# Kernel optimization log

Measured on AMD Instinct MI355X. Metric: run time of the kernel, lower is better.

The kernel has to match this reference:

```python
import jax, jax.numpy as jnp
import numpy as np

E, H, I, T, K = 8, 2048, 1024, 4096, 2
GROUP = 32


def dequant_int4(packed, scale, group):
    """packed: [E, R, C//2] ints in [0,256) holding two 4-bit values per byte.
    scale: [E, R, C//group]. Returns fp32 [E, R, C] with w = (nibble - 8) * scale."""
    lo = (packed & 0xF) - 8          # even columns
    hi = ((packed >> 4) & 0xF) - 8   # odd columns
    e, r, ch = packed.shape
    w = jnp.stack([lo, hi], axis=-1).reshape(e, r, 2 * ch).astype(jnp.float32)
    w = w.reshape(e, r, -1, group) * scale[..., None]
    return w.reshape(e, r, 2 * ch)


def setup_inputs() -> dict:
    key = jax.random.key(0)
    ks = jax.random.split(key, 6)
    x = jax.random.normal(ks[0], (T, H), dtype=jnp.float32)
    w1 = jax.random.randint(ks[1], (E, 2 * I, H // 2), 0, 256, dtype=jnp.int32)
    w1_scale = jax.random.uniform(ks[2], (E, 2 * I, H // GROUP), dtype=jnp.float32) * 0.02
    w2 = jax.random.randint(ks[3], (E, H, I // 2), 0, 256, dtype=jnp.int32)
    w2_scale = jax.random.uniform(ks[4], (E, H, I // GROUP), dtype=jnp.float32) * 0.02
    logits = jax.random.normal(ks[5], (T, E), dtype=jnp.float32)
    top_vals, top_idx = jax.lax.top_k(logits, K)
    expert_weights = jax.nn.softmax(top_vals, axis=-1)   # [T, K]
    expert_indices = top_idx.astype(jnp.int32)           # [T, K]
    return {"x": x, "w1": w1, "w1_scale": w1_scale, "w2": w2,
            "w2_scale": w2_scale, "expert_weights": expert_weights,
            "expert_indices": expert_indices, "top_k": K}


def reference(x, w1, w1_scale, w2, w2_scale, expert_weights, expert_indices, top_k):
    inter = w2.shape[2] * 2
    W1 = dequant_int4(w1, w1_scale, GROUP)   # [E, 2I, H]
    W2 = dequant_int4(w2, w2_scale, GROUP)   # [E, H, I]
    y13 = jnp.einsum('th,erh->etr', x, W1)   # [E, T, 2I]
    gate, up = y13[..., :inter], y13[..., inter:]
    h = jax.nn.silu(gate) * up               # [E, T, I] SwiGLU
    y = jnp.einsum('eti,ehi->eth', h, W2)    # [E, T, H]
    t_ids = jnp.arange(x.shape[0])[:, None]  # [T, 1]
    sel = y[expert_indices, t_ids, :]        # [T, K, H]
    return jnp.einsum('tkh,tk->th', sel, expert_weights)
```

## Files before the change

kernel.cpp:

```cpp
#include <hip/hip_runtime.h>
#include <cstdint>
#include <cstddef>

typedef unsigned int u32;
typedef unsigned short u16;
typedef __bf16 bf16x8 __attribute__((ext_vector_type(8)));
typedef float f32x4 __attribute__((ext_vector_type(4)));
typedef u16 u16x8 __attribute__((ext_vector_type(8)));

static constexpr int T_TOK = 4096;
static constexpr int HID   = 2048;
static constexpr int INTER = 1024;
static constexpr int NEXP  = 8;
static constexpr int TOPK  = 2;
static constexpr int SLOT_CAP = 10240;
static constexpr int NT_M = 40;

static constexpr int M_TOT    = 16;
static constexpr int M_CUR    = 17;
static constexpr int M_DONE   = 40;
static constexpr int M_TOK    = 96;
static constexpr int M_SLOTOF = 96 + SLOT_CAP;

__device__ __forceinline__ u16 f2bf(float f) {
  u32 u = __builtin_bit_cast(u32, f);
  u32 r = (u + 0x7fffu + ((u >> 16) & 1u)) >> 16;
  return (u16)r;
}
__device__ __forceinline__ float bf2f(u16 h) {
  return __builtin_bit_cast(float, (u32)h << 16);
}

__device__ __forceinline__ void spin_ge(int* p, int target) {
  while (__hip_atomic_load(p, __ATOMIC_RELAXED, __HIP_MEMORY_SCOPE_AGENT) < target)
    __builtin_amdgcn_s_sleep(8);
  __builtin_amdgcn_fence(__ATOMIC_ACQUIRE, "agent");
}
__device__ __forceinline__ void bump(int* p, int tid) {
  __syncthreads();
  if (tid == 0)
    __hip_atomic_fetch_add(p, 1, __ATOMIC_RELEASE, __HIP_MEMORY_SCOPE_AGENT);
}

__global__ void router_count(const int* __restrict__ eidx, int* __restrict__ meta) {
  __shared__ int cnt[NEXP];
  const int tid = threadIdx.x;
  if (tid < NEXP) cnt[tid] = 0;
  __syncthreads();
  for (int i = tid; i < T_TOK * TOPK; i += 256) atomicAdd(&cnt[eidx[i]], 1);
  __syncthreads();
  if (tid == 0) {
    int off = 0;
    for (int e = 0; e < NEXP; ++e) {
      int c = cnt[e];
      meta[e] = c;
      meta[8 + e] = off;
      meta[M_CUR + e] = off;
      off += (c + 255) & ~255;
    }
    meta[M_TOT] = off;
  }
}

__global__ void init_k(int* __restrict__ meta) {
  const int i = blockIdx.x * 256 + threadIdx.x;
  if (i < SLOT_CAP) meta[M_TOK + i] = 0;
  if (i >= 25 && i < 80) meta[i] = 0;
}

__global__ void router_assign(const int* __restrict__ eidx, int* __restrict__ meta) {
  const int t = blockIdx.x * 256 + threadIdx.x;
  if (t >= T_TOK) return;
  int* cursors = meta + M_CUR;
  int* toklist = meta + M_TOK;
  int* slotof  = meta + M_SLOTOF;
  for (int k = 0; k < TOPK; ++k) {
    const int e = eidx[t * TOPK + k];
    const int pos = atomicAdd(&cursors[e], 1);
    toklist[pos] = t * 2 + k;
    slotof[t * 2 + k] = pos;
  }
}

template <int CPR>
__device__ __forceinline__ void deq1(const int* __restrict__ p, const float* __restrict__ s,
                                     u16* __restrict__ w, int gid) {
  const int row = gid / CPR;
  const int cid = gid % CPR;
  const int4 pk = *(const int4*)(p + (size_t)gid * 4);
  const float sc = s[(size_t)row * (CPR / 4) + (cid >> 2)];
  int v[4] = {pk.x, pk.y, pk.z, pk.w};
  u16x8 o;
#pragma unroll
  for (int b = 0; b < 4; ++b) {
    o[2 * b]     = f2bf((float)((v[b] & 15) - 8) * sc);
    o[2 * b + 1] = f2bf((float)(((v[b] >> 4) & 15) - 8) * sc);
  }
  *(u16x8*)(w + (size_t)gid * 8) = o;
}

__global__ void prep_k(const int* __restrict__ w1, const float* __restrict__ w1s,
                       const int* __restrict__ w2, const float* __restrict__ w2s,
                       const float* __restrict__ x, u16* __restrict__ W1b,
                       u16* __restrict__ W2b, u16* __restrict__ xs,
                       const int* __restrict__ meta) {
  const int blk = blockIdx.x;
  if (blk < 16384) {
    deq1<256>(w1, w1s, W1b, blk * 256 + threadIdx.x);
  } else if (blk < 24576) {
    deq1<128>(w2, w2s, W2b, (blk - 16384) * 256 + threadIdx.x);
  } else {
    const int slot = blk - 24576;
    const int tok = meta[M_TOK + slot] >> 1;
    const float* src = x + (size_t)tok * HID + threadIdx.x * 8;
    const float4 a = *(const float4*)src;
    const float4 b = *(const float4*)(src + 4);
    u16x8 o;
    o[0] = f2bf(a.x); o[1] = f2bf(a.y); o[2] = f2bf(a.z); o[3] = f2bf(a.w);
    o[4] = f2bf(b.x); o[5] = f2bf(b.y); o[6] = f2bf(b.z); o[7] = f2bf(b.w);
    *(u16x8*)(xs + (size_t)slot * HID + threadIdx.x * 8) = o;
  }
}

template <int KT, bool G1M>
__device__ void gemm_body(const u16* __restrict__ A, const u16* __restrict__ Be,
                          u16* __restrict__ Cout, u16* lds, int slot0, int nt, int tid) {
  static constexpr int NT = KT / 64;
  char* ldsB = (char*)lds;

  const u16* asrc[4];
  const u16* bsrc[4];
#pragma unroll
  for (int j = 0; j < 4; ++j) {
    const int L = j * 8192 + tid * 16;
    const int S = L >> 10;
    int o = L & 1023;
    o ^= ((o >> 7) & 3) << 4;
    const int r = (S >> 1) * 16 + (o >> 6);
    const int cb = (S & 1) * 64 + (o & 63);
    asrc[j] = A + (size_t)(slot0 + r) * KT + (cb >> 1);
    int brow;
    if (G1M) {
      const int g = r >> 6, j6 = r & 63;
      brow = nt * 128 + g * 32 + (j6 & 31) + ((j6 >> 5) << 10);
    } else {
      brow = nt * 256 + r;
    }
    bsrc[j] = Be + (size_t)brow * KT + (cb >> 1);
  }

#define STAGE(kt_, c_)                                                                \
  do {                                                                                \
    char* dA_ = ldsB + (c_) * 65536;                                                  \
    char* dB_ = dA_ + 32768;                                                          \
    _Pragma("unroll") for (int j = 0; j < 4; ++j)                                     \
        __builtin_amdgcn_global_load_lds(                                             \
            (const __attribute__((address_space(1))) void*)(asrc[j] + (kt_) * 64),    \
            (__attribute__((address_space(3))) void*)(dA_ + j * 8192 + tid * 16),     \
            16, 0, 0);                                                                \
    _Pragma("unroll") for (int j = 0; j < 4; ++j)                                     \
        __builtin_amdgcn_global_load_lds(                                             \
            (const __attribute__((address_space(1))) void*)(bsrc[j] + (kt_) * 64),    \
            (__attribute__((address_space(3))) void*)(dB_ + j * 8192 + tid * 16),     \
            16, 0, 0);                                                                \
  } while (0)

  const int lane = tid & 63;
  const int wid = tid >> 6;
  const int wm = (wid >> 2) * 128;
  const int wn = (wid & 3) * 64;
  const int fr = lane & 15;
  const int qq = lane >> 4;
  const int swz = (qq * 16) ^ (((fr >> 1) & 3) << 4);

  const int abase = (wm >> 4) * 2048 + fr * 64 + swz;
  const int bbase = 32768 + (wn >> 4) * 2048 + fr * 64 + swz;

  f32x4 acc[8][4];
#pragma unroll
  for (int m = 0; m < 8; ++m)
#pragma unroll
    for (int n = 0; n < 4; ++n) acc[m][n] = (f32x4)0.0f;

#define COMPUTE(c_)                                                                   \
  do {                                                                                \
    const char* bb_ = ldsB + (c_) * 65536;                                            \
    bf16x8 bfr_[4][2];                                                                \
    _Pragma("unroll") for (int nf = 0; nf < 4; ++nf)                                  \
        _Pragma("unroll") for (int ks = 0; ks < 2; ++ks)                              \
            bfr_[nf][ks] = *(const bf16x8*)(bb_ + bbase + nf * 2048 + ks * 1024);     \
    _Pragma("unroll") for (int mh = 0; mh < 2; ++mh) {                                \
      bf16x8 af_[4][2];                                                               \
      _Pragma("unroll") for (int mf = 0; mf < 4; ++mf)                                \
          _Pragma("unroll") for (int ks = 0; ks < 2; ++ks)                            \
              af_[mf][ks] = *(const bf16x8*)(bb_ + abase + mh * 8192 + mf * 2048 +    \
                                             ks * 1024);                              \
      __builtin_amdgcn_s_setprio(1);                                                  \
      _Pragma("unroll") for (int mf = 0; mf < 4; ++mf)                                \
          _Pragma("unroll") for (int nf = 0; nf < 4; ++nf)                            \
              _Pragma("unroll") for (int ks = 0; ks < 2; ++ks)                        \
                  acc[mh * 4 + mf][nf] = __builtin_amdgcn_mfma_f32_16x16x32_bf16(     \
                      af_[mf][ks], bfr_[nf][ks], acc[mh * 4 + mf][nf], 0, 0, 0);      \
      __builtin_amdgcn_s_setprio(0);                                                  \
    }                                                                                 \
  } while (0)

  STAGE(0, 0);
#pragma unroll 1
  for (int kt = 0; kt < NT; kt += 2) {
    asm volatile("s_waitcnt vmcnt(0)" ::: "memory");
    __builtin_amdgcn_s_barrier();
    __builtin_amdgcn_sched_barrier(0);
    if (kt + 1 < NT) STAGE(kt + 1, 1);
    COMPUTE(0);
    asm volatile("s_waitcnt vmcnt(0)" ::: "memory");
    __builtin_amdgcn_s_barrier();
    __builtin_amdgcn_sched_barrier(0);
    if (kt + 2 < NT) STAGE(kt + 2, 0);
    COMPUTE(1);
  }
#undef STAGE
#undef COMPUTE

  if (G1M) {
    const int g = wid & 3;
#pragma unroll
    for (int mi = 0; mi < 8; ++mi)
#pragma unroll
      for (int n = 0; n < 2; ++n)
#pragma unroll
        for (int jj = 0; jj < 4; ++jj) {
          const float gv = acc[mi][n][jj];
          const float uv = acc[mi][n + 2][jj];
          const float hv = gv / (1.0f + __expf(-gv)) * uv;
          const int row = slot0 + wm + mi * 16 + qq * 4 + jj;
          Cout[(size_t)row * INTER + nt * 128 + g * 32 + n * 16 + fr] = f2bf(hv);
        }
  } else {
#pragma unroll
    for (int mi = 0; mi < 8; ++mi)
#pragma unroll
      for (int jj = 0; jj < 4; ++jj) {
        const int row = slot0 + wm + mi * 16 + qq * 4 + jj;
        const int col = nt * 256 + wn + fr;
#pragma unroll
        for (int n = 0; n < 4; ++n)
          Cout[(size_t)row * HID + col + n * 16] = f2bf(acc[mi][n][jj]);
      }
  }
}

__device__ __forceinline__ void run_g1(const u16* xs, const u16* W1b, u16* hbuf,
                                       int* meta, u16* lds, int mt, int nt, int tid) {
  const int slot0 = mt * 256;
  if (slot0 < meta[M_TOT]) {
    int e = 0;
#pragma unroll
    for (int i = 1; i < NEXP; ++i) e += (slot0 >= meta[8 + i]);
    gemm_body<2048, true>(xs, W1b + (size_t)e * 2048 * 2048, hbuf, lds, slot0, nt, tid);
  }
  bump(&meta[M_DONE + mt], tid);
}

__device__ __forceinline__ void run_g2(const u16* hbuf, const u16* W2b, u16* ys,
                                       int* meta, u16* lds, int mt, int nt, int tid) {
  const int slot0 = mt * 256;
  if (slot0 >= meta[M_TOT]) return;
  int e = 0;
#pragma unroll
  for (int i = 1; i < NEXP; ++i) e += (slot0 >= meta[8 + i]);
  if (tid == 0) spin_ge(&meta[M_DONE + mt], 8);
  __syncthreads();
  gemm_body<1024, false>(hbuf, W2b + (size_t)e * 2048 * 1024, ys, lds, slot0, nt, tid);
}

__global__ __launch_bounds__(512, 2) void gemm_static(
    const u16* __restrict__ xs, const u16* __restrict__ W1b,
    const u16* __restrict__ W2b, u16* __restrict__ hbuf, u16* __restrict__ ys,
    int* __restrict__ meta) {
  __shared__ u16 lds[2 * 32768];
  const int tid = threadIdx.x;
  const int b = blockIdx.x;

  run_g1(xs, W1b, hbuf, meta, lds, b & 31, b >> 5, tid);
  if (b < 64) {
    run_g1(xs, W1b, hbuf, meta, lds, 32 + (b & 7), b >> 3, tid);
    run_g2(hbuf, W2b, ys, meta, lds, 32 + (b & 7), b >> 3, tid);
  } else {
    const int x = b & 7, q = (b - 64) >> 3;
    {
      const int k = q;
      run_g2(hbuf, W2b, ys, meta, lds, x + 8 * (k & 3), k >> 2, tid);
    }
    if (q < 8) {
      const int k = q + 24;
      run_g2(hbuf, W2b, ys, meta, lds, x + 8 * (k & 3), k >> 2, tid);
    }
  }
}

__global__ void combine_k(const u16* __restrict__ ys, const float* __restrict__ ew,
                          const int* __restrict__ meta, float* __restrict__ out) {
  const int idx = blockIdx.x * 256 + threadIdx.x;
  const int t = idx >> 8;
  const int pos = (idx & 255) * 8;
  const int* slotof = meta + M_SLOTOF;
  const int s0 = slotof[t * 2];
  const int s1 = slotof[t * 2 + 1];
  const float w0 = ew[t * 2];
  const float w1 = ew[t * 2 + 1];
  const u16x8 v0 = *(const u16x8*)(ys + (size_t)s0 * HID + pos);
  const u16x8 v1 = *(const u16x8*)(ys + (size_t)s1 * HID + pos);
  float* dst = out + (size_t)t * HID + pos;
  float4 o0, o1;
  o0.x = w0 * bf2f(v0[0]) + w1 * bf2f(v1[0]);
  o0.y = w0 * bf2f(v0[1]) + w1 * bf2f(v1[1]);
  o0.z = w0 * bf2f(v0[2]) + w1 * bf2f(v1[2]);
  o0.w = w0 * bf2f(v0[3]) + w1 * bf2f(v1[3]);
  o1.x = w0 * bf2f(v0[4]) + w1 * bf2f(v1[4]);
  o1.y = w0 * bf2f(v0[5]) + w1 * bf2f(v1[5]);
  o1.z = w0 * bf2f(v0[6]) + w1 * bf2f(v1[6]);
  o1.w = w0 * bf2f(v0[7]) + w1 * bf2f(v1[7]);
  *(float4*)dst = o0;
  *(float4*)(dst + 4) = o1;
}

extern "C" void kernel_launch(void* const* d_in, const int* in_sizes, int n_in,
                              void* d_out, int out_size, void* d_ws, size_t ws_size,
                              hipStream_t stream) {
  const float* x    = (const float*)d_in[0];
  const int*   w1   = (const int*)d_in[1];
  const float* w1s  = (const float*)d_in[2];
  const int*   w2   = (const int*)d_in[3];
  const float* w2s  = (const float*)d_in[4];
  const float* ew   = (const float*)d_in[5];
  const int*   eidx = (const int*)d_in[6];
  float* out = (float*)d_out;

  char* ws = (char*)d_ws;
  const size_t OFF_W1B  = 0;
  const size_t OFF_W2B  = 67108864;
  const size_t OFF_XS   = 100663296;
  const size_t OFF_H    = 142606336;
  const size_t OFF_META = 163577856;
  const size_t NEED     = 163708928;
  if (ws_size < NEED) return;

  u16* W1b  = (u16*)(ws + OFF_W1B);
  u16* W2b  = (u16*)(ws + OFF_W2B);
  u16* xs   = (u16*)(ws + OFF_XS);
  u16* hbuf = (u16*)(ws + OFF_H);
  int* meta = (int*)(ws + OFF_META);

  router_count<<<1, 256, 0, stream>>>(eidx, meta);
  init_k<<<SLOT_CAP / 256, 256, 0, stream>>>(meta);
  router_assign<<<T_TOK / 256, 256, 0, stream>>>(eidx, meta);

  prep_k<<<34816, 256, 0, stream>>>(w1, w1s, w2, w2s, x, W1b, W2b, xs, meta);

  gemm_static<<<256, 512, 0, stream>>>(xs, W1b, W2b, hbuf, xs, meta);

  combine_k<<<(T_TOK * HID) / (256 * 8), 256, 0, stream>>>(xs, ew, meta, out);
}
```

Baseline: 254.3 us.

## Fuse int4 weight dequant into GEMM B-tile staging, drop prep pass

Removes the separate pass that dequantized all expert weights to bf16 in workspace. The GEMM now loads packed int4 words and scales into registers, dequantizes them, and writes bf16 B tiles directly into LDS, with a reworked double-buffer schedule. The x gather becomes a per-token kernel that writes each token's bf16 row to both of its slots. This saves the large bf16 weight write and reread, but adds VALU dequant work and register pressure inside the GEMM loop, and B loads lose the async global-to-LDS path. Each weight tile is also dequantized once per M-tile rather than once overall.

```diff
diff --git a/kernel.cpp b/kernel.cpp
--- a/kernel.cpp
+++ b/kernel.cpp
@@ -82,54 +82,33 @@
   }
 }
 
-template <int CPR>
-__device__ __forceinline__ void deq1(const int* __restrict__ p, const float* __restrict__ s,
-                                     u16* __restrict__ w, int gid) {
-  const int row = gid / CPR;
-  const int cid = gid % CPR;
-  const int4 pk = *(const int4*)(p + (size_t)gid * 4);
-  const float sc = s[(size_t)row * (CPR / 4) + (cid >> 2)];
-  int v[4] = {pk.x, pk.y, pk.z, pk.w};
+__global__ void xprep_k(const float* __restrict__ x, const int* __restrict__ meta,
+                        u16* __restrict__ xs) {
+  const int t = blockIdx.x;
+  const int col = threadIdx.x * 8;
+  const float* src = x + (size_t)t * HID + col;
+  const float4 a = *(const float4*)src;
+  const float4 b = *(const float4*)(src + 4);
   u16x8 o;
-#pragma unroll
-  for (int b = 0; b < 4; ++b) {
-    o[2 * b]     = f2bf((float)((v[b] & 15) - 8) * sc);
-    o[2 * b + 1] = f2bf((float)(((v[b] >> 4) & 15) - 8) * sc);
-  }
-  *(u16x8*)(w + (size_t)gid * 8) = o;
-}
-
-__global__ void prep_k(const int* __restrict__ w1, const float* __restrict__ w1s,
-                       const int* __restrict__ w2, const float* __restrict__ w2s,
-                       const float* __restrict__ x, u16* __restrict__ W1b,
-                       u16* __restrict__ W2b, u16* __restrict__ xs,
-                       const int* __restrict__ meta) {
-  const int blk = blockIdx.x;
-  if (blk < 16384) {
-    deq1<256>(w1, w1s, W1b, blk * 256 + threadIdx.x);
-  } else if (blk < 24576) {
-    deq1<128>(w2, w2s, W2b, (blk - 16384) * 256 + threadIdx.x);
-  } else {
-    const int slot = blk - 24576;
-    const int tok = meta[M_TOK + slot] >> 1;
-    const float* src = x + (size_t)tok * HID + threadIdx.x * 8;
-    const float4 a = *(const float4*)src;
-    const float4 b = *(const float4*)(src + 4);
-    u16x8 o;
-    o[0] = f2bf(a.x); o[1] = f2bf(a.y); o[2] = f2bf(a.z); o[3] = f2bf(a.w);
-    o[4] = f2bf(b.x); o[5] = f2bf(b.y); o[6] = f2bf(b.z); o[7] = f2bf(b.w);
-    *(u16x8*)(xs + (size_t)slot * HID + threadIdx.x * 8) = o;
-  }
+  o[0] = f2bf(a.x); o[1] = f2bf(a.y); o[2] = f2bf(a.z); o[3] = f2bf(a.w);
+  o[4] = f2bf(b.x); o[5] = f2bf(b.y); o[6] = f2bf(b.z); o[7] = f2bf(b.w);
+  const int s0 = meta[M_SLOTOF + 2 * t];
+  const int s1 = meta[M_SLOTOF + 2 * t + 1];
+  *(u16x8*)(xs + (size_t)s0 * HID + col) = o;
+  *(u16x8*)(xs + (size_t)s1 * HID + col) = o;
 }
 
 template <int KT, bool G1M>
-__device__ void gemm_body(const u16* __restrict__ A, const u16* __restrict__ Be,
-                          u16* __restrict__ Cout, u16* lds, int slot0, int nt, int tid) {
+__device__ void gemm_body(const u16* __restrict__ A, const int* __restrict__ Wp,
+                          const float* __restrict__ Ws, u16* __restrict__ Cout,
+                          u16* lds, int slot0, int nt, int tid) {
   static constexpr int NT = KT / 64;
   char* ldsB = (char*)lds;
 
   const u16* asrc[4];
-  const u16* bsrc[4];
+  const int4* bpk[4];
+  const float* bsp[4];
+  int bdst[4];
 #pragma unroll
   for (int j = 0; j < 4; ++j) {
     const int L = j * 8192 + tid * 16;
@@ -146,24 +125,44 @@
     } else {
       brow = nt * 256 + r;
     }
-    bsrc[j] = Be + (size_t)brow * KT + (cb >> 1);
-  }
-
-#define STAGE(kt_, c_)                                                                \
+    bpk[j] = (const int4*)(Wp + (size_t)brow * (KT / 2) + (cb >> 2));
+    bsp[j] = Ws + (size_t)brow * (KT / 32) + (S & 1);
+    bdst[j] = 32768 + L;
+  }
+
+#define STAGE_A(kt_, c_)                                                              \
   do {                                                                                \
-    char* dA_ = ldsB + (c_) * 65536;                                                  \
-    char* dB_ = dA_ + 32768;                                                          \
     _Pragma("unroll") for (int j = 0; j < 4; ++j)                                     \
         __builtin_amdgcn_global_load_lds(                                             \
             (const __attribute__((address_space(1))) void*)(asrc[j] + (kt_) * 64),    \
-            (__attribute__((address_space(3))) void*)(dA_ + j * 8192 + tid * 16),     \
-            16, 0, 0);                                                                \
-    _Pragma("unroll") for (int j = 0; j < 4; ++j)                                     \
-        __builtin_amdgcn_global_load_lds(                                             \
-            (const __attribute__((address_space(1))) void*)(bsrc[j] + (kt_) * 64),    \
-            (__attribute__((address_space(3))) void*)(dB_ + j * 8192 + tid * 16),     \
+            (__attribute__((address_space(3))) void*)(ldsB + (c_) * 65536 +           \
+                                                     j * 8192 + tid * 16),            \
             16, 0, 0);                                                                \
   } while (0)
+
+  int4 pk0, pk1, pk2, pk3;
+  float sc0, sc1, sc2, sc3;
+#define B_LOAD(kt_)                                                                   \
+  do {                                                                               \
+    pk0 = bpk[0][(kt_) * 8]; sc0 = bsp[0][(kt_) * 2];                                \
+    pk1 = bpk[1][(kt_) * 8]; sc1 = bsp[1][(kt_) * 2];                                \
+    pk2 = bpk[2][(kt_) * 8]; sc2 = bsp[2][(kt_) * 2];                                \
+    pk3 = bpk[3][(kt_) * 8]; sc3 = bsp[3][(kt_) * 2];                                \
+  } while (0)
+
+#define BW1(c_, pk_, sc_, j_)                                                         \
+  do {                                                                               \
+    const int v_[4] = {pk_.x, pk_.y, pk_.z, pk_.w};                                  \
+    u16x8 q_;                                                                        \
+    _Pragma("unroll") for (int b = 0; b < 4; ++b) {                                  \
+      q_[2 * b]     = f2bf((float)((v_[b] & 15) - 8) * sc_);                         \
+      q_[2 * b + 1] = f2bf((float)(((v_[b] >> 4) & 15) - 8) * sc_);                  \
+    }                                                                                \
+    *(u16x8*)(ldsB + (c_) * 65536 + bdst[j_]) = q_;                                  \
+  } while (0)
+#define B_WRITE(c_)                                                                   \
+  do { BW1(c_, pk0, sc0, 0); BW1(c_, pk1, sc1, 1);                                   \
+       BW1(c_, pk2, sc2, 2); BW1(c_, pk3, sc3, 3); } while (0)
 
   const int lane = tid & 63;
   const int wid = tid >> 6;
@@ -205,21 +204,43 @@
     }                                                                                 \
   } while (0)
 
-  STAGE(0, 0);
+  STAGE_A(0, 0);
+  B_LOAD(0);
+  asm volatile("s_waitcnt vmcnt(0)" ::: "memory");
+  __builtin_amdgcn_sched_barrier(0);
+  B_WRITE(0);
+  asm volatile("s_waitcnt lgkmcnt(0)" ::: "memory");
+  __builtin_amdgcn_s_barrier();
+
 #pragma unroll 1
   for (int kt = 0; kt < NT; kt += 2) {
+    STAGE_A(kt + 1, 1);
+    B_LOAD(kt + 1);
+    __builtin_amdgcn_sched_barrier(0);
+    COMPUTE(0);
+    __builtin_amdgcn_sched_barrier(0);
     asm volatile("s_waitcnt vmcnt(0)" ::: "memory");
+    B_WRITE(1);
+    asm volatile("s_waitcnt lgkmcnt(0)" ::: "memory");
     __builtin_amdgcn_s_barrier();
+    if (kt + 2 < NT) {
+      STAGE_A(kt + 2, 0);
+      B_LOAD(kt + 2);
+    }
     __builtin_amdgcn_sched_barrier(0);
-    if (kt + 1 < NT) STAGE(kt + 1, 1);
-    COMPUTE(0);
+    COMPUTE(1);
+    __builtin_amdgcn_sched_barrier(0);
     asm volatile("s_waitcnt vmcnt(0)" ::: "memory");
+    if (kt + 2 < NT) {
+      B_WRITE(0);
+      asm volatile("s_waitcnt lgkmcnt(0)" ::: "memory");
+    }
     __builtin_amdgcn_s_barrier();
-    __builtin_amdgcn_sched_barrier(0);
-    if (kt + 2 < NT) STAGE(kt + 2, 0);
-    COMPUTE(1);
-  }
-#undef STAGE
+  }
+#undef STAGE_A
+#undef B_LOAD
+#undef BW1
+#undef B_WRITE
 #undef COMPUTE
 
   if (G1M) {
@@ -250,20 +271,23 @@
   }
 }
 
-__device__ __forceinline__ void run_g1(const u16* xs, const u16* W1b, u16* hbuf,
-                                       int* meta, u16* lds, int mt, int nt, int tid) {
+__device__ __forceinline__ void run_g1(const u16* xs, const int* w1, const float* w1s,
+                                       u16* hbuf, int* meta, u16* lds,
+                                       int mt, int nt, int tid) {
   const int slot0 = mt * 256;
   if (slot0 < meta[M_TOT]) {
     int e = 0;
 #pragma unroll
     for (int i = 1; i < NEXP; ++i) e += (slot0 >= meta[8 + i]);
-    gemm_body<2048, true>(xs, W1b + (size_t)e * 2048 * 2048, hbuf, lds, slot0, nt, tid);
+    gemm_body<2048, true>(xs, w1 + (size_t)e * 2048 * 1024,
+                          w1s + (size_t)e * 2048 * 64, hbuf, lds, slot0, nt, tid);
   }
   bump(&meta[M_DONE + mt], tid);
 }
 
-__device__ __forceinline__ void run_g2(const u16* hbuf, const u16* W2b, u16* ys,
-                                       int* meta, u16* lds, int mt, int nt, int tid) {
+__device__ __forceinline__ void run_g2(const u16* hbuf, const int* w2, const float* w2s,
+                                       u16* ys, int* meta, u16* lds,
+                                       int mt, int nt, int tid) {
   const int slot0 = mt * 256;
   if (slot0 >= meta[M_TOT]) return;
   int e = 0;
@@ -271,30 +295,32 @@
   for (int i = 1; i < NEXP; ++i) e += (slot0 >= meta[8 + i]);
   if (tid == 0) spin_ge(&meta[M_DONE + mt], 8);
   __syncthreads();
-  gemm_body<1024, false>(hbuf, W2b + (size_t)e * 2048 * 1024, ys, lds, slot0, nt, tid);
+  gemm_body<1024, false>(hbuf, w2 + (size_t)e * 2048 * 512,
+                         w2s + (size_t)e * 2048 * 32, ys, lds, slot0, nt, tid);
 }
 
 __global__ __launch_bounds__(512, 2) void gemm_static(
-    const u16* __restrict__ xs, const u16* __restrict__ W1b,
-    const u16* __restrict__ W2b, u16* __restrict__ hbuf, u16* __restrict__ ys,
+    const u16* __restrict__ xs, const int* __restrict__ w1,
+    const float* __restrict__ w1s, const int* __restrict__ w2,
+    const float* __restrict__ w2s, u16* __restrict__ hbuf, u16* __restrict__ ys,
     int* __restrict__ meta) {
   __shared__ u16 lds[2 * 32768];
   const int tid = threadIdx.x;
   const int b = blockIdx.x;
 
-  run_g1(xs, W1b, hbuf, meta, lds, b & 31, b >> 5, tid);
+  run_g1(xs, w1, w1s, hbuf, meta, lds, b & 31, b >> 5, tid);
   if (b < 64) {
-    run_g1(xs, W1b, hbuf, meta, lds, 32 + (b & 7), b >> 3, tid);
-    run_g2(hbuf, W2b, ys, meta, lds, 32 + (b & 7), b >> 3, tid);
+    run_g1(xs, w1, w1s, hbuf, meta, lds, 32 + (b & 7), b >> 3, tid);
+    run_g2(hbuf, w2, w2s, ys, meta, lds, 32 + (b & 7), b >> 3, tid);
   } else {
     const int x = b & 7, q = (b - 64) >> 3;
     {
       const int k = q;
-      run_g2(hbuf, W2b, ys, meta, lds, x + 8 * (k & 3), k >> 2, tid);
+      run_g2(hbuf, w2, w2s, ys, meta, lds, x + 8 * (k & 3), k >> 2, tid);
     }
     if (q < 8) {
       const int k = q + 24;
-      run_g2(hbuf, W2b, ys, meta, lds, x + 8 * (k & 3), k >> 2, tid);
+      run_g2(hbuf, w2, w2s, ys, meta, lds, x + 8 * (k & 3), k >> 2, tid);
     }
   }
 }
@@ -338,16 +364,12 @@
   float* out = (float*)d_out;
 
   char* ws = (char*)d_ws;
-  const size_t OFF_W1B  = 0;
-  const size_t OFF_W2B  = 67108864;
-  const size_t OFF_XS   = 100663296;
-  const size_t OFF_H    = 142606336;
-  const size_t OFF_META = 163577856;
-  const size_t NEED     = 163708928;
+  const size_t OFF_XS   = 0;
+  const size_t OFF_H    = 41943040;
+  const size_t OFF_META = 62914560;
+  const size_t NEED     = 63045632;
   if (ws_size < NEED) return;
 
-  u16* W1b  = (u16*)(ws + OFF_W1B);
-  u16* W2b  = (u16*)(ws + OFF_W2B);
   u16* xs   = (u16*)(ws + OFF_XS);
   u16* hbuf = (u16*)(ws + OFF_H);
   int* meta = (int*)(ws + OFF_META);
@@ -356,9 +378,9 @@
   init_k<<<SLOT_CAP / 256, 256, 0, stream>>>(meta);
   router_assign<<<T_TOK / 256, 256, 0, stream>>>(eidx, meta);
 
-  prep_k<<<34816, 256, 0, stream>>>(w1, w1s, w2, w2s, x, W1b, W2b, xs, meta);
-
-  gemm_static<<<256, 512, 0, stream>>>(xs, W1b, W2b, hbuf, xs, meta);
+  xprep_k<<<T_TOK, 256, 0, stream>>>(x, meta, xs);
+
+  gemm_static<<<256, 512, 0, stream>>>(xs, w1, w1s, w2, w2s, hbuf, xs, meta);
 
   combine_k<<<(T_TOK * HID) / (256 * 8), 256, 0, stream>>>(xs, ew, meta, out);
 }
```

After: 428.6 us. 68.5% more time.
